# Kernel optimization log

Hardware: AMD Instinct MI355X
Metric: run time of the kernel (lower is better)

Reference implementation:

```python
import jax, jax.numpy as jnp
import numpy as np

DN = ('NCHW', 'OIHW', 'NCHW')


def conv2d(x, w, b, pad=1):
    y = jax.lax.conv_general_dilated(x, w, window_strides=(1, 1),
                                     padding=[(pad, pad), (pad, pad)],
                                     dimension_numbers=DN)
    return y + b[None, :, None, None]


def deform_conv2d(x, offset, w, b):
    """Deformable conv v1 (torchvision layout): offset [B, 2*K*K, H, W],
    channel 2k = dy_k, 2k+1 = dx_k, kernel points row-major."""
    B, C, H, W = x.shape
    K = 3
    off = offset.reshape(B, K * K, 2, H, W)
    dy, dx = off[:, :, 0], off[:, :, 1]            # [B,9,H,W]
    ky = jnp.repeat(jnp.arange(K) - 1, K).astype(x.dtype)   # row-major kernel grid
    kx = jnp.tile(jnp.arange(K) - 1, K).astype(x.dtype)
    hh = jnp.arange(H, dtype=x.dtype)
    ww = jnp.arange(W, dtype=x.dtype)
    py = hh[None, None, :, None] + ky[None, :, None, None] + dy  # [B,9,H,W]
    px = ww[None, None, None, :] + kx[None, :, None, None] + dx

    y0 = jnp.floor(py)
    x0 = jnp.floor(px)
    ly, lx = py - y0, px - x0
    y0i, x0i = y0.astype(jnp.int32), x0.astype(jnp.int32)

    def gather(yi, xi):
        valid = ((yi >= 0) & (yi < H) & (xi >= 0) & (xi < W))
        yc = jnp.clip(yi, 0, H - 1)
        xc = jnp.clip(xi, 0, W - 1)
        # per-batch fancy gather: [C,H,W] indexed by [9,H,W] -> [C,9,H,W]
        g = jax.vmap(lambda xb, yy, xx: xb[:, yy, xx])(x, yc, xc)  # [B,C,9,H,W]
        return g * valid[:, None].astype(x.dtype)

    w00 = ((1 - ly) * (1 - lx))[:, None]
    w01 = ((1 - ly) * lx)[:, None]
    w10 = (ly * (1 - lx))[:, None]
    w11 = (ly * lx)[:, None]
    val = (gather(y0i, x0i) * w00 + gather(y0i, x0i + 1) * w01 +
           gather(y0i + 1, x0i) * w10 + gather(y0i + 1, x0i + 1) * w11)  # [B,C,9,H,W]

    wk = w.reshape(w.shape[0], C * K * K)                 # [Cout, C*9]
    out = jnp.einsum('bkhw,ok->bohw', val.reshape(B, C * K * K, H, W), wk)
    return out + b[None, :, None, None]


def setup_inputs() -> dict:
    key = jax.random.key(0)
    k1, k2, k3, k4 = jax.random.split(key, 4)
    B, Cin, Cout, H, W = 8, 128, 256, 64, 64
    fan = 1.0 / np.sqrt(Cin * 9)
    return {
        'x': jax.random.normal(k1, (B, Cin, H, W), jnp.float32),
        'w_off': jax.random.normal(k2, (18, Cin, 3, 3), jnp.float32) * 0.01,
        'b_off': jnp.zeros((18,), jnp.float32),
        'w_def': jax.random.normal(k3, (Cout, Cin, 3, 3), jnp.float32) * fan,
        'b_def': jax.random.normal(k4, (Cout,), jnp.float32) * 0.01,
    }


def reference(x, w_off, b_off, w_def, b_def):
    offset = conv2d(x, w_off, b_off, pad=1)
    y = deform_conv2d(x, offset, w_def, b_def)
    return jax.nn.relu(y)
```

## Files before the change

kernel.cpp:

```cpp
#include <hip/hip_runtime.h>
#include <hip/hip_bf16.h>

#define HH 64
#define WW 64
#define CIN 128
#define COUT 256
#define KK 1152
#define PW 66
#define XTIMG (PW*PW*CIN)

typedef short bf16x8 __attribute__((ext_vector_type(8)));
typedef float f32x4  __attribute__((ext_vector_type(4)));

__device__ inline short f2bf(float f) {
    union { float f; unsigned u; } v; v.f = f;
    unsigned r = v.u + 0x7FFFu + ((v.u >> 16) & 1u);
    return (short)(r >> 16);
}
__device__ inline float lo16(unsigned u) {
    union { unsigned u; float f; } v; v.u = u << 16; return v.f;
}
__device__ inline float hi16(unsigned u) {
    union { unsigned u; float f; } v; v.u = u & 0xffff0000u; return v.f;
}
__device__ inline unsigned pk2(float lo, float hi) {
    union { __hip_bfloat162 h; unsigned u; } c;
    c.h = __float22bfloat162_rn(make_float2(lo, hi));
    return c.u;
}

__global__ __launch_bounds__(256) void prep(const float* __restrict__ x,
                                            const float* __restrict__ wd,
                                            const float* __restrict__ wo,
                                            ushort* __restrict__ xt,
                                            short* __restrict__ wf,
                                            short* __restrict__ wfo) {
    int bi = blockIdx.x, t = threadIdx.x;
    if (bi >= 528) {
        int flat = (bi - 528) * 256 + t;
        int m = flat / 2304;
        int r = flat - m * 2304;
        int ks = r >> 6, l = r & 63;
        bf16x8 v;
        if (m < 16) {
            int co = m * 16 + (l & 15);
#pragma unroll
            for (int j = 0; j < 8; j++) {
                int ckp = ks * 32 + ((l >> 4) << 3) + j;
                int c = ckp & 127, k = ckp >> 7;
                v[j] = f2bf(wd[(size_t)co * KK + c * 9 + k]);
            }
            *(bf16x8*)(wf + ((size_t)(m * 36 + ks) * 64 + l) * 8) = v;
        } else {
            int mm = m - 16;
            int co = mm * 16 + (l & 15);
#pragma unroll
            for (int j = 0; j < 8; j++) {
                int ckp = ks * 32 + ((l >> 4) << 3) + j;
                int c = ckp & 127, k = ckp >> 7;
                v[j] = (co < 18) ? f2bf(wo[(size_t)co * KK + c * 9 + k]) : (short)0;
            }
            *(bf16x8*)(wfo + ((size_t)(mm * 36 + ks) * 64 + l) * 8) = v;
        }
        return;
    }
    int hp = bi % 66, b = bi / 66;
    ushort* row = xt + ((size_t)b * PW + hp) * PW * CIN;
    if (hp == 0 || hp == PW - 1) {
        ushort4 z4 = {0, 0, 0, 0};
        for (int f = t; f < 2112; f += 256) ((ushort4*)row)[f] = z4;
        return;
    }
    __shared__ short tl[66 * 132];
    int h = hp - 1;
    if (t < 128) { tl[t] = 0; tl[65 * 132 + t] = 0; }
    const float* xbh = x + (((size_t)b * CIN) << 12) + (h << 6);
#pragma unroll
    for (int it = 0; it < 8; it++) {
        int c  = it * 16 + (t >> 4);
        int w4 = (t & 15) * 4;
        float4 v = *(const float4*)(xbh + ((size_t)c << 12) + w4);
        tl[(w4 + 1) * 132 + c] = f2bf(v.x);
        tl[(w4 + 2) * 132 + c] = f2bf(v.y);
        tl[(w4 + 3) * 132 + c] = f2bf(v.z);
        tl[(w4 + 4) * 132 + c] = f2bf(v.w);
    }
    __syncthreads();
    for (int f = t; f < 2112; f += 256) {
        int wp = f >> 5, c4 = (f & 31) * 4;
        const short* s = &tl[wp * 132 + c4];
        ushort4 v; v.x = s[0]; v.y = s[1]; v.z = s[2]; v.w = s[3];
        ((ushort4*)row)[f] = v;
    }
}

__global__ __launch_bounds__(256, 2) void fused_deform(const ushort* __restrict__ xt,
                                                       const short* __restrict__ wf,
                                                       const short* __restrict__ wfo,
                                                       const float* __restrict__ bo,
                                                       const float* __restrict__ bias,
                                                       float* __restrict__ out) {
    __shared__ short   s_val[64][128];
    __shared__ float4  s_w[9][64];
    __shared__ ushort2 s_o[9][64];
    __shared__ float   s_off[18][64];

    int t = threadIdx.x, bi = blockIdx.x;
    int b = bi & 7, h = bi >> 3;
    const ushort* xb = xt + (size_t)b * XTIMG;
    int wv = t >> 6, l = t & 63, lane16 = l & 15, quad = l >> 4;

    {
        f32x4 aoff0 = {0.f, 0.f, 0.f, 0.f}, aoff1 = aoff0;
        const short* A0 = wfo + (size_t)l * 8;
        const short* A1 = wfo + (size_t)36 * 512 + l * 8;
        int pix0 = lane16 + 16 * wv;
#pragma unroll 1
        for (int k = 0; k < 9; k++) {
            const ushort* bbase = xb + ((size_t)(h + k / 3) * PW + pix0 + k % 3) * CIN + quad * 8;
#pragma unroll
            for (int ksp = 0; ksp < 4; ksp++) {
                int ks = k * 4 + ksp;
                bf16x8 bfr = *(const bf16x8*)(bbase + ksp * 32);
                bf16x8 af0 = *(const bf16x8*)(A0 + (size_t)ks * 512);
                bf16x8 af1 = *(const bf16x8*)(A1 + (size_t)ks * 512);
                aoff0 = __builtin_amdgcn_mfma_f32_16x16x32_bf16(af0, bfr, aoff0, 0, 0, 0);
                aoff1 = __builtin_amdgcn_mfma_f32_16x16x32_bf16(af1, bfr, aoff1, 0, 0, 0);
            }
        }
#pragma unroll
        for (int r = 0; r < 4; r++) {
            int co = quad * 4 + r;
            s_off[co][pix0] = aoff0[r] + bo[co];
            int co1 = co + 16;
            if (co1 < 18) s_off[co1][pix0] = aoff1[r] + bo[co1];
        }
    }
    __syncthreads();

    for (int jj = t; jj < 576; jj += 256) {
        int k = jj >> 6, pixj = jj & 63, wp = pixj;
        float dy = s_off[2 * k][pixj];
        float dx = s_off[2 * k + 1][pixj];
        float py = (float)(h + k / 3 - 1) + dy;
        float px = (float)(wp + k % 3 - 1) + dx;
        float y0f = floorf(py), x0f = floorf(px);
        float ly = py - y0f, lx = px - x0f;
        int y0 = (int)y0f, x0 = (int)x0f;
        float a0, a1;
        if (x0 >= 0 && x0 <= 62)      { a0 = 1.f - lx; a1 = lx; }
        else if (x0 == -1)            { a0 = lx;       a1 = 0.f; }
        else if (x0 == 63)            { a0 = 0.f;      a1 = 1.f - lx; }
        else                          { a0 = 0.f;      a1 = 0.f; }
        int xb0 = min(max(x0, 0), 62);
        bool vy0 = (y0 >= 0) && (y0 < HH);
        bool vy1 = (y0 >= -1) && (y0 < HH - 1);
        int y0c = min(max(y0, 0), HH - 1);
        int y1c = min(max(y0 + 1, 0), HH - 1);
        float wy0 = (1.f - ly) * (vy0 ? 1.f : 0.f);
        float wy1 = ly * (vy1 ? 1.f : 0.f);
        s_o[k][pixj] = make_ushort2((ushort)((y0c + 1) * PW + xb0 + 1),
                                    (ushort)((y1c + 1) * PW + xb0 + 1));
        s_w[k][pixj] = make_float4(wy0 * a0, wy0 * a1, wy1 * a0, wy1 * a1);
    }

    int gpix = t >> 2, sub = t & 3;
    const ushort* xg = xb + sub * 8;
    bf16x8 cur[4];

    auto gli = [&](int k) {
        ushort2 o = s_o[k][gpix];
        float4 w4 = s_w[k][gpix];
        const ushort* p0 = xg + (size_t)o.x * CIN;
        const ushort* p1 = xg + (size_t)o.y * CIN;
        uint4 c00[4], c01[4], c10[4], c11[4];
#pragma unroll
        for (int i = 0; i < 4; i++) {
            c00[i] = *(const uint4*)(p0 + i * 32);
            c01[i] = *(const uint4*)(p0 + 128 + i * 32);
            c10[i] = *(const uint4*)(p1 + i * 32);
            c11[i] = *(const uint4*)(p1 + 128 + i * 32);
        }
#pragma unroll
        for (int i = 0; i < 4; i++) {
            uint4 o4;
            const unsigned* u00 = (const unsigned*)&c00[i];
            const unsigned* u01 = (const unsigned*)&c01[i];
            const unsigned* u10 = (const unsigned*)&c10[i];
            const unsigned* u11 = (const unsigned*)&c11[i];
            unsigned* ov = (unsigned*)&o4;
#pragma unroll
            for (int d = 0; d < 4; d++) {
                float vl = w4.x * lo16(u00[d]) + w4.y * lo16(u01[d])
                         + w4.z * lo16(u10[d]) + w4.w * lo16(u11[d]);
                float vh = w4.x * hi16(u00[d]) + w4.y * hi16(u01[d])
                         + w4.z * hi16(u10[d]) + w4.w * hi16(u11[d]);
                ov[d] = pk2(vl, vh);
            }
            cur[i] = *(bf16x8*)&o4;
        }
    };

    f32x4 z = {0.f, 0.f, 0.f, 0.f};
    f32x4 acc[4][4];
#pragma unroll
    for (int i = 0; i < 4; i++)
#pragma unroll
        for (int j = 0; j < 4; j++) acc[i][j] = z;
    const short* Aw = wf + (size_t)l * 8;

    __syncthreads();
    gli(0);

    for (int k = 0; k < 9; k++) {
#pragma unroll
        for (int i = 0; i < 4; i++)
            *(bf16x8*)&s_val[gpix][((((i << 2) + sub) ^ (gpix & 15)) << 3)] = cur[i];
        __syncthreads();
        if (k < 8) gli(k + 1);
#pragma unroll
        for (int ksp = 0; ksp < 4; ksp++) {
            int ks = k * 4 + ksp;
            int gg = (ksp << 2) + quad;
            bf16x8 b0 = *(const bf16x8*)&s_val[lane16     ][(gg ^ lane16) << 3];
            bf16x8 b1 = *(const bf16x8*)&s_val[16 + lane16][(gg ^ lane16) << 3];
            bf16x8 b2 = *(const bf16x8*)&s_val[32 + lane16][(gg ^ lane16) << 3];
            bf16x8 b3 = *(const bf16x8*)&s_val[48 + lane16][(gg ^ lane16) << 3];
#pragma unroll
            for (int mt = 0; mt < 4; mt++) {
                bf16x8 a = *(const bf16x8*)(Aw + (size_t)(((wv * 4 + mt) * 36) + ks) * 512);
                acc[mt][0] = __builtin_amdgcn_mfma_f32_16x16x32_bf16(a, b0, acc[mt][0], 0, 0, 0);
                acc[mt][1] = __builtin_amdgcn_mfma_f32_16x16x32_bf16(a, b1, acc[mt][1], 0, 0, 0);
                acc[mt][2] = __builtin_amdgcn_mfma_f32_16x16x32_bf16(a, b2, acc[mt][2], 0, 0, 0);
                acc[mt][3] = __builtin_amdgcn_mfma_f32_16x16x32_bf16(a, b3, acc[mt][3], 0, 0, 0);
            }
        }
        __syncthreads();
    }

#pragma unroll
    for (int mt = 0; mt < 4; mt++) {
        int co = (wv * 4 + mt) * 16 + quad * 4;
#pragma unroll
        for (int nt = 0; nt < 4; nt++) {
            int colx = nt * 16 + lane16;
#pragma unroll
            for (int rr = 0; rr < 4; rr++) {
                float v = acc[mt][nt][rr] + bias[co + rr];
                out[(((size_t)b * COUT + co + rr) << 12) + (h << 6) + colx] = fmaxf(v, 0.f);
            }
        }
    }
}

extern "C" void kernel_launch(void* const* d_in, const int* in_sizes, int n_in,
                              void* d_out, int out_size, void* d_ws, size_t ws_size,
                              hipStream_t stream) {
    const float* x     = (const float*)d_in[0];
    const float* w_off = (const float*)d_in[1];
    const float* b_off = (const float*)d_in[2];
    const float* w_def = (const float*)d_in[3];
    const float* b_def = (const float*)d_in[4];
    float* out = (float*)d_out;

    short*  wf  = (short*)d_ws;
    short*  wfo = wf + (size_t)16 * 36 * 512;
    ushort* xt  = (ushort*)(wfo + (size_t)2 * 36 * 512);

    prep<<<690, 256, 0, stream>>>(x, w_def, w_off, xt, wf, wfo);
    fused_deform<<<512, 256, 0, stream>>>(xt, wf, wfo, b_off, b_def, out);
}
```

Measured before the change: 140.5 us.

## Double-buffer deform gather, use 512-thread blocks, rewrite prep transpose without LDS

The main kernel moves to 512 threads per block. Each wave now owns two output-channel tiles instead of four, and the offset conv is split across 8 waves. The sampled-value LDS tile is double-buffered: the next tap's global loads are issued before the MFMAs and the bilinear blend is stored afterwards, which removes one barrier per tap and overlaps gather latency with compute. Separately, the prep kernel transposes x to NHWC bf16 with direct per-thread strided loads and packed stores instead of going through a shared-memory tile. The risks are higher register pressure from 8 held vectors plus occupancy targets, and strided uncoalesced reads in prep.

```diff
diff --git a/kernel.cpp b/kernel.cpp
--- a/kernel.cpp
+++ b/kernel.cpp
@@ -36,71 +36,67 @@
                                             short* __restrict__ wf,
                                             short* __restrict__ wfo) {
     int bi = blockIdx.x, t = threadIdx.x;
-    if (bi >= 528) {
-        int flat = (bi - 528) * 256 + t;
-        int m = flat / 2304;
-        int r = flat - m * 2304;
-        int ks = r >> 6, l = r & 63;
-        bf16x8 v;
-        if (m < 16) {
-            int co = m * 16 + (l & 15);
-#pragma unroll
-            for (int j = 0; j < 8; j++) {
-                int ckp = ks * 32 + ((l >> 4) << 3) + j;
-                int c = ckp & 127, k = ckp >> 7;
-                v[j] = f2bf(wd[(size_t)co * KK + c * 9 + k]);
-            }
-            *(bf16x8*)(wf + ((size_t)(m * 36 + ks) * 64 + l) * 8) = v;
-        } else {
-            int mm = m - 16;
-            int co = mm * 16 + (l & 15);
-#pragma unroll
-            for (int j = 0; j < 8; j++) {
-                int ckp = ks * 32 + ((l >> 4) << 3) + j;
-                int c = ckp & 127, k = ckp >> 7;
-                v[j] = (co < 18) ? f2bf(wo[(size_t)co * KK + c * 9 + k]) : (short)0;
-            }
-            *(bf16x8*)(wfo + ((size_t)(mm * 36 + ks) * 64 + l) * 8) = v;
+    if (bi < 528) {
+        int b = bi & 7, hp = bi >> 3;
+        ushort* row = xt + ((size_t)b * PW + hp) * PW * CIN;
+        if (hp == 0 || hp == 65) {
+            uint4 z = {0, 0, 0, 0};
+            for (int f = t; f < 1056; f += 256) ((uint4*)row)[f] = z;
+            return;
+        }
+        int h = hp - 1;
+        int w = t & 63, c0 = (t >> 6) * 32;
+        const float* xs = x + (((size_t)b * CIN + c0) << 12) + (h << 6) + w;
+        float v[32];
+#pragma unroll
+        for (int i = 0; i < 32; i++) v[i] = xs[(size_t)i << 12];
+        unsigned dw[16];
+#pragma unroll
+        for (int i = 0; i < 16; i++) dw[i] = pk2(v[2 * i], v[2 * i + 1]);
+        ushort* dst = row + ((w + 1) * 128 + c0);
+#pragma unroll
+        for (int i = 0; i < 4; i++) *(uint4*)(dst + i * 8) = *(uint4*)&dw[i * 4];
+        if (t < 32) {
+            uint4 z = {0, 0, 0, 0};
+            int px = (t >> 4) * 65;
+            *(uint4*)(row + px * 128 + (t & 15) * 8) = z;
         }
         return;
     }
-    int hp = bi % 66, b = bi / 66;
-    ushort* row = xt + ((size_t)b * PW + hp) * PW * CIN;
-    if (hp == 0 || hp == PW - 1) {
-        ushort4 z4 = {0, 0, 0, 0};
-        for (int f = t; f < 2112; f += 256) ((ushort4*)row)[f] = z4;
-        return;
-    }
-    __shared__ short tl[66 * 132];
-    int h = hp - 1;
-    if (t < 128) { tl[t] = 0; tl[65 * 132 + t] = 0; }
-    const float* xbh = x + (((size_t)b * CIN) << 12) + (h << 6);
-#pragma unroll
-    for (int it = 0; it < 8; it++) {
-        int c  = it * 16 + (t >> 4);
-        int w4 = (t & 15) * 4;
-        float4 v = *(const float4*)(xbh + ((size_t)c << 12) + w4);
-        tl[(w4 + 1) * 132 + c] = f2bf(v.x);
-        tl[(w4 + 2) * 132 + c] = f2bf(v.y);
-        tl[(w4 + 3) * 132 + c] = f2bf(v.z);
-        tl[(w4 + 4) * 132 + c] = f2bf(v.w);
-    }
-    __syncthreads();
-    for (int f = t; f < 2112; f += 256) {
-        int wp = f >> 5, c4 = (f & 31) * 4;
-        const short* s = &tl[wp * 132 + c4];
-        ushort4 v; v.x = s[0]; v.y = s[1]; v.z = s[2]; v.w = s[3];
-        ((ushort4*)row)[f] = v;
-    }
-}
-
-__global__ __launch_bounds__(256, 2) void fused_deform(const ushort* __restrict__ xt,
+    int flat = (bi - 528) * 256 + t;
+    int m = flat / 2304;
+    int r = flat - m * 2304;
+    int ks = r >> 6, l = r & 63;
+    bf16x8 v8;
+    if (m < 16) {
+        int co = m * 16 + (l & 15);
+#pragma unroll
+        for (int j = 0; j < 8; j++) {
+            int ckp = ks * 32 + ((l >> 4) << 3) + j;
+            int c = ckp & 127, k = ckp >> 7;
+            v8[j] = f2bf(wd[(size_t)co * KK + c * 9 + k]);
+        }
+        *(bf16x8*)(wf + ((size_t)(m * 36 + ks) * 64 + l) * 8) = v8;
+    } else {
+        int mm = m - 16;
+        int co = mm * 16 + (l & 15);
+#pragma unroll
+        for (int j = 0; j < 8; j++) {
+            int ckp = ks * 32 + ((l >> 4) << 3) + j;
+            int c = ckp & 127, k = ckp >> 7;
+            v8[j] = (co < 18) ? f2bf(wo[(size_t)co * KK + c * 9 + k]) : (short)0;
+        }
+        *(bf16x8*)(wfo + ((size_t)(mm * 36 + ks) * 64 + l) * 8) = v8;
+    }
+}
+
+__global__ __launch_bounds__(512, 4) void fused_deform(const ushort* __restrict__ xt,
                                                        const short* __restrict__ wf,
                                                        const short* __restrict__ wfo,
                                                        const float* __restrict__ bo,
                                                        const float* __restrict__ bias,
                                                        float* __restrict__ out) {
-    __shared__ short   s_val[64][128];
+    __shared__ short   s_val[2][64][128];
     __shared__ float4  s_w[9][64];
     __shared__ ushort2 s_o[9][64];
     __shared__ float   s_off[18][64];
@@ -111,39 +107,34 @@
     int wv = t >> 6, l = t & 63, lane16 = l & 15, quad = l >> 4;
 
     {
-        f32x4 aoff0 = {0.f, 0.f, 0.f, 0.f}, aoff1 = aoff0;
-        const short* A0 = wfo + (size_t)l * 8;
-        const short* A1 = wfo + (size_t)36 * 512 + l * 8;
-        int pix0 = lane16 + 16 * wv;
-#pragma unroll 1
+        int mt = wv >> 2, nt = wv & 3;
+        int pix0 = nt * 16 + lane16;
+        f32x4 aoff = {0.f, 0.f, 0.f, 0.f};
+        const short* A = wfo + (size_t)mt * 36 * 512 + l * 8;
+#pragma unroll
         for (int k = 0; k < 9; k++) {
             const ushort* bbase = xb + ((size_t)(h + k / 3) * PW + pix0 + k % 3) * CIN + quad * 8;
 #pragma unroll
             for (int ksp = 0; ksp < 4; ksp++) {
-                int ks = k * 4 + ksp;
                 bf16x8 bfr = *(const bf16x8*)(bbase + ksp * 32);
-                bf16x8 af0 = *(const bf16x8*)(A0 + (size_t)ks * 512);
-                bf16x8 af1 = *(const bf16x8*)(A1 + (size_t)ks * 512);
-                aoff0 = __builtin_amdgcn_mfma_f32_16x16x32_bf16(af0, bfr, aoff0, 0, 0, 0);
-                aoff1 = __builtin_amdgcn_mfma_f32_16x16x32_bf16(af1, bfr, aoff1, 0, 0, 0);
+                bf16x8 afr = *(const bf16x8*)(A + (k * 4 + ksp) * 512);
+                aoff = __builtin_amdgcn_mfma_f32_16x16x32_bf16(afr, bfr, aoff, 0, 0, 0);
             }
         }
 #pragma unroll
         for (int r = 0; r < 4; r++) {
-            int co = quad * 4 + r;
-            s_off[co][pix0] = aoff0[r] + bo[co];
-            int co1 = co + 16;
-            if (co1 < 18) s_off[co1][pix0] = aoff1[r] + bo[co1];
+            int co = mt * 16 + quad * 4 + r;
+            if (co < 18) s_off[co][pix0] = aoff[r] + bo[co];
         }
     }
     __syncthreads();
 
-    for (int jj = t; jj < 576; jj += 256) {
-        int k = jj >> 6, pixj = jj & 63, wp = pixj;
+    for (int jj = t; jj < 576; jj += 512) {
+        int k = jj >> 6, pixj = jj & 63;
         float dy = s_off[2 * k][pixj];
         float dx = s_off[2 * k + 1][pixj];
         float py = (float)(h + k / 3 - 1) + dy;
-        float px = (float)(wp + k % 3 - 1) + dx;
+        float px = (float)(pixj + k % 3 - 1) + dx;
         float y0f = floorf(py), x0f = floorf(px);
         float ly = py - y0f, lx = px - x0f;
         int y0 = (int)y0f, x0 = (int)x0f;
@@ -164,89 +155,88 @@
         s_w[k][pixj] = make_float4(wy0 * a0, wy0 * a1, wy1 * a0, wy1 * a1);
     }
 
-    int gpix = t >> 2, sub = t & 3;
-    const ushort* xg = xb + sub * 8;
-    bf16x8 cur[4];
-
-    auto gli = [&](int k) {
-        ushort2 o = s_o[k][gpix];
-        float4 w4 = s_w[k][gpix];
-        const ushort* p0 = xg + (size_t)o.x * CIN;
-        const ushort* p1 = xg + (size_t)o.y * CIN;
-        uint4 c00[4], c01[4], c10[4], c11[4];
-#pragma unroll
-        for (int i = 0; i < 4; i++) {
-            c00[i] = *(const uint4*)(p0 + i * 32);
-            c01[i] = *(const uint4*)(p0 + 128 + i * 32);
-            c10[i] = *(const uint4*)(p1 + i * 32);
-            c11[i] = *(const uint4*)(p1 + 128 + i * 32);
-        }
-#pragma unroll
-        for (int i = 0; i < 4; i++) {
-            uint4 o4;
-            const unsigned* u00 = (const unsigned*)&c00[i];
-            const unsigned* u01 = (const unsigned*)&c01[i];
-            const unsigned* u10 = (const unsigned*)&c10[i];
-            const unsigned* u11 = (const unsigned*)&c11[i];
-            unsigned* ov = (unsigned*)&o4;
-#pragma unroll
-            for (int d = 0; d < 4; d++) {
-                float vl = w4.x * lo16(u00[d]) + w4.y * lo16(u01[d])
-                         + w4.z * lo16(u10[d]) + w4.w * lo16(u11[d]);
-                float vh = w4.x * hi16(u00[d]) + w4.y * hi16(u01[d])
-                         + w4.z * hi16(u10[d]) + w4.w * hi16(u11[d]);
-                ov[d] = pk2(vl, vh);
-            }
-            cur[i] = *(bf16x8*)&o4;
-        }
+    int p = t >> 3, j = t & 7, c0 = j * 16;
+    int g0 = ((2 * j) ^ (p & 15)) * 8, g1 = ((2 * j + 1) ^ (p & 15)) * 8;
+    bf16x8 rv[8];
+    auto gload = [&](int k) {
+        ushort2 o = s_o[k][p];
+        const ushort* p0 = xb + (size_t)o.x * CIN + c0;
+        const ushort* p1 = xb + (size_t)o.y * CIN + c0;
+        rv[0] = *(const bf16x8*)(p0);       rv[1] = *(const bf16x8*)(p0 + 8);
+        rv[2] = *(const bf16x8*)(p0 + 128); rv[3] = *(const bf16x8*)(p0 + 136);
+        rv[4] = *(const bf16x8*)(p1);       rv[5] = *(const bf16x8*)(p1 + 8);
+        rv[6] = *(const bf16x8*)(p1 + 128); rv[7] = *(const bf16x8*)(p1 + 136);
     };
+    auto gstore = [&](int k, int buf) {
+        float4 w4 = s_w[k][p];
+        unsigned oa[4], ob[4];
+        const unsigned* u0 = (const unsigned*)&rv[0];
+        const unsigned* u2 = (const unsigned*)&rv[2];
+        const unsigned* u4 = (const unsigned*)&rv[4];
+        const unsigned* u6 = (const unsigned*)&rv[6];
+        const unsigned* u1 = (const unsigned*)&rv[1];
+        const unsigned* u3 = (const unsigned*)&rv[3];
+        const unsigned* u5 = (const unsigned*)&rv[5];
+        const unsigned* u7 = (const unsigned*)&rv[7];
+#pragma unroll
+        for (int d = 0; d < 4; d++) {
+            float vl = w4.x * lo16(u0[d]) + w4.y * lo16(u2[d]) + w4.z * lo16(u4[d]) + w4.w * lo16(u6[d]);
+            float vh = w4.x * hi16(u0[d]) + w4.y * hi16(u2[d]) + w4.z * hi16(u4[d]) + w4.w * hi16(u6[d]);
+            oa[d] = pk2(vl, vh);
+            float wl = w4.x * lo16(u1[d]) + w4.y * lo16(u3[d]) + w4.z * lo16(u5[d]) + w4.w * lo16(u7[d]);
+            float wh = w4.x * hi16(u1[d]) + w4.y * hi16(u3[d]) + w4.z * hi16(u5[d]) + w4.w * hi16(u7[d]);
+            ob[d] = pk2(wl, wh);
+        }
+        *(bf16x8*)&s_val[buf][p][g0] = *(bf16x8*)oa;
+        *(bf16x8*)&s_val[buf][p][g1] = *(bf16x8*)ob;
+    };
 
     f32x4 z = {0.f, 0.f, 0.f, 0.f};
-    f32x4 acc[4][4];
-#pragma unroll
-    for (int i = 0; i < 4; i++)
-#pragma unroll
-        for (int j = 0; j < 4; j++) acc[i][j] = z;
-    const short* Aw = wf + (size_t)l * 8;
+    f32x4 acc[2][4];
+#pragma unroll
+    for (int i = 0; i < 2; i++)
+#pragma unroll
+        for (int jj2 = 0; jj2 < 4; jj2++) acc[i][jj2] = z;
+    const short* Aw = wf + (size_t)l * 8 + (size_t)(wv * 2) * 36 * 512;
 
     __syncthreads();
-    gli(0);
+    gload(0); gstore(0, 0);
+    __syncthreads();
 
     for (int k = 0; k < 9; k++) {
-#pragma unroll
-        for (int i = 0; i < 4; i++)
-            *(bf16x8*)&s_val[gpix][((((i << 2) + sub) ^ (gpix & 15)) << 3)] = cur[i];
-        __syncthreads();
-        if (k < 8) gli(k + 1);
+        if (k < 8) gload(k + 1);
 #pragma unroll
         for (int ksp = 0; ksp < 4; ksp++) {
             int ks = k * 4 + ksp;
-            int gg = (ksp << 2) + quad;
-            bf16x8 b0 = *(const bf16x8*)&s_val[lane16     ][(gg ^ lane16) << 3];
-            bf16x8 b1 = *(const bf16x8*)&s_val[16 + lane16][(gg ^ lane16) << 3];
-            bf16x8 b2 = *(const bf16x8*)&s_val[32 + lane16][(gg ^ lane16) << 3];
-            bf16x8 b3 = *(const bf16x8*)&s_val[48 + lane16][(gg ^ lane16) << 3];
-#pragma unroll
-            for (int mt = 0; mt < 4; mt++) {
-                bf16x8 a = *(const bf16x8*)(Aw + (size_t)(((wv * 4 + mt) * 36) + ks) * 512);
-                acc[mt][0] = __builtin_amdgcn_mfma_f32_16x16x32_bf16(a, b0, acc[mt][0], 0, 0, 0);
-                acc[mt][1] = __builtin_amdgcn_mfma_f32_16x16x32_bf16(a, b1, acc[mt][1], 0, 0, 0);
-                acc[mt][2] = __builtin_amdgcn_mfma_f32_16x16x32_bf16(a, b2, acc[mt][2], 0, 0, 0);
-                acc[mt][3] = __builtin_amdgcn_mfma_f32_16x16x32_bf16(a, b3, acc[mt][3], 0, 0, 0);
-            }
-        }
+            int gsw = ((ksp * 4 + quad) ^ lane16) * 8;
+            bf16x8 b0 = *(const bf16x8*)&s_val[k & 1][lane16     ][gsw];
+            bf16x8 b1 = *(const bf16x8*)&s_val[k & 1][16 + lane16][gsw];
+            bf16x8 b2 = *(const bf16x8*)&s_val[k & 1][32 + lane16][gsw];
+            bf16x8 b3 = *(const bf16x8*)&s_val[k & 1][48 + lane16][gsw];
+            bf16x8 a0 = *(const bf16x8*)(Aw + (size_t)(0 * 36 + ks) * 512);
+            bf16x8 a1 = *(const bf16x8*)(Aw + (size_t)(1 * 36 + ks) * 512);
+            acc[0][0] = __builtin_amdgcn_mfma_f32_16x16x32_bf16(a0, b0, acc[0][0], 0, 0, 0);
+            acc[0][1] = __builtin_amdgcn_mfma_f32_16x16x32_bf16(a0, b1, acc[0][1], 0, 0, 0);
+            acc[0][2] = __builtin_amdgcn_mfma_f32_16x16x32_bf16(a0, b2, acc[0][2], 0, 0, 0);
+            acc[0][3] = __builtin_amdgcn_mfma_f32_16x16x32_bf16(a0, b3, acc[0][3], 0, 0, 0);
+            acc[1][0] = __builtin_amdgcn_mfma_f32_16x16x32_bf16(a1, b0, acc[1][0], 0, 0, 0);
+            acc[1][1] = __builtin_amdgcn_mfma_f32_16x16x32_bf16(a1, b1, acc[1][1], 0, 0, 0);
+            acc[1][2] = __builtin_amdgcn_mfma_f32_16x16x32_bf16(a1, b2, acc[1][2], 0, 0, 0);
+            acc[1][3] = __builtin_amdgcn_mfma_f32_16x16x32_bf16(a1, b3, acc[1][3], 0, 0, 0);
+        }
+        if (k < 8) gstore(k + 1, (k + 1) & 1);
         __syncthreads();
     }
 
 #pragma unroll
-    for (int mt = 0; mt < 4; mt++) {
-        int co = (wv * 4 + mt) * 16 + quad * 4;
+    for (int mt2 = 0; mt2 < 2; mt2++) {
+        int co = (wv * 2 + mt2) * 16 + quad * 4;
 #pragma unroll
         for (int nt = 0; nt < 4; nt++) {
             int colx = nt * 16 + lane16;
 #pragma unroll
             for (int rr = 0; rr < 4; rr++) {
-                float v = acc[mt][nt][rr] + bias[co + rr];
+                float v = acc[mt2][nt][rr] + bias[co + rr];
                 out[(((size_t)b * COUT + co + rr) << 12) + (h << 6) + colx] = fmaxf(v, 0.f);
             }
         }
@@ -268,5 +258,5 @@
     ushort* xt  = (ushort*)(wfo + (size_t)2 * 36 * 512);
 
     prep<<<690, 256, 0, stream>>>(x, w_def, w_off, xt, wf, wfo);
-    fused_deform<<<512, 256, 0, stream>>>(xt, wf, wfo, b_off, b_def, out);
-}
+    fused_deform<<<512, 512, 0, stream>>>(xt, wf, wfo, b_off, b_def, out);
+}
```

After: 135.0 us. 1.04x faster.
